# Kernel tuning notes

Hardware: AMD Instinct MI355X
Metric: run time of the kernel (lower is better)

The kernel has to match this reference:

```python
import math
import jax, jax.numpy as jnp
import numpy as np

V_NODES = 100000
N_EDGES = 1600000
EMBED = 768
HID = 256
H = 4
FH = HID // H
L = 2
PE_D = EMBED // 4  # 192
SLOPE = 0.2


def make_pe(max_len, d):
    pos = np.arange(max_len, dtype=np.float32)[:, None]
    div = np.exp(np.arange(0, d, 2, dtype=np.float32) * (-math.log(10000.0) / d))
    pe = np.zeros((max_len, d), dtype=np.float32)
    pe[:, 0::2] = np.sin(pos * div)
    pe[:, 1::2] = np.cos(pos * div)
    return jnp.asarray(pe)


def setup_inputs() -> dict:
    key = jax.random.key(0)
    ks = jax.random.split(key, 24)

    def xavier(k, shape):
        fan_in, fan_out = shape[0], shape[1]
        lim = math.sqrt(6.0 / (fan_in + fan_out))
        return jax.random.uniform(k, shape, jnp.float32, -lim, lim)

    in_proj_dim = EMBED + 2 * PE_D  # 1152
    inp = {
        'row_idx': jax.random.randint(ks[0], (V_NODES,), 0, 256),
        'col_idx': jax.random.randint(ks[1], (V_NODES,), 0, 64),
        'edge_index': jax.random.randint(ks[2], (2, N_EDGES), 0, V_NODES),
        'edge_weight': jax.random.uniform(ks[3], (N_EDGES,), jnp.float32),
        'W_in': xavier(ks[4], (in_proj_dim, HID)),
        'b_in': jnp.zeros((HID,), jnp.float32),
        'ln_g': jnp.ones((HID,), jnp.float32),
        'ln_b': jnp.zeros((HID,), jnp.float32),
        'Wq': jnp.stack([xavier(ks[5 + i], (HID, HID)) for i in range(L)]),
        'bq': jnp.zeros((L, HID), jnp.float32),
        'Wk': jnp.stack([xavier(ks[7 + i], (HID, HID)) for i in range(L)]),
        'bk': jnp.zeros((L, HID), jnp.float32),
        'Wv': jnp.stack([xavier(ks[9 + i], (HID, HID)) for i in range(L)]),
        'bv': jnp.zeros((L, HID), jnp.float32),
        'Wo': jnp.stack([xavier(ks[11 + i], (HID, HID)) for i in range(L)]),
        'bo': jnp.zeros((L, HID), jnp.float32),
        'We': jnp.stack([xavier(ks[13 + i], (1, H)) for i in range(L)]),  # edge_proj weight [1,H]
        'be': jnp.zeros((L, H), jnp.float32),
    }
    return inp


def gat_layer(h, src, tgt, ew, Wq, bq, Wk, bk, Wv, bv, Wo, bo, We, be):
    V = h.shape[0]
    Q = (h @ Wq + bq).reshape(V, H, FH)
    K = (h @ Wk + bk).reshape(V, H, FH)
    Vo = (h @ Wv + bv).reshape(V, H, FH)
    # edge bias: Linear(1,H) on edge_weight, then leaky relu -> [E,H]
    edge_bias = jax.nn.leaky_relu(ew[:, None] * We.reshape(1, H) + be, SLOPE)
    attn_raw = jnp.sum(Q[src] * K[tgt], axis=-1) / math.sqrt(FH) + edge_bias  # [E,H]
    attn_exp = jnp.exp(attn_raw)
    deg = jax.ops.segment_sum(attn_exp, tgt, num_segments=V) + 1e-16  # [V,H]
    attn_norm = attn_exp / deg[tgt]  # [E,H] (dropout is identity at eval)
    msg = Vo[src] * attn_norm[:, :, None] * ew[:, None, None]  # [E,H,FH]
    out = jax.ops.segment_sum(msg, tgt, num_segments=V).reshape(V, H * FH)
    return jax.nn.leaky_relu(out @ Wo + bo, SLOPE)


def reference(row_idx, col_idx, edge_index, edge_weight,
              W_in, b_in, ln_g, ln_b,
              Wq, bq, Wk, bk, Wv, bv, Wo, bo, We, be):
    V = row_idx.shape[0]
    row_pe = make_pe(256, PE_D)
    col_pe = make_pe(64, PE_D)
    cell = jnp.zeros((V, EMBED), jnp.float32)  # cell_embeds are zeros in source
    h = jnp.concatenate([cell, row_pe[row_idx], col_pe[col_idx]], axis=-1)
    # input_proj: Linear -> LayerNorm -> ReLU (dropout identity)
    h = h @ W_in + b_in
    mu = jnp.mean(h, axis=-1, keepdims=True)
    var = jnp.var(h, axis=-1, keepdims=True)
    h = (h - mu) / jnp.sqrt(var + 1e-5) * ln_g + ln_b
    h = jax.nn.relu(h)
    src, tgt = edge_index[0], edge_index[1]
    for i in range(L):
        h = gat_layer(h, src, tgt, edge_weight,
                      Wq[i], bq[i], Wk[i], bk[i], Wv[i], bv[i],
                      Wo[i], bo[i], We[i], be[i])
    return h
```

## Files before the change

### kernel.cpp

```cpp
#include <hip/hip_runtime.h>
#include <hip/hip_bf16.h>
#include <type_traits>
#include <math.h>

typedef __attribute__((ext_vector_type(8))) short bf16x8;
typedef __attribute__((ext_vector_type(4))) float f32x4;

__device__ __forceinline__ float bf2f(unsigned int u16) {
    union { unsigned int i; float f; } x; x.i = (u16 & 0xffffu) << 16; return x.f;
}
__device__ __forceinline__ unsigned int f2bf(float f) {
    union { float f; unsigned int i; } x; x.f = f;
    unsigned int i = x.i;
    unsigned int r = i + 0x7fffu + ((i >> 16) & 1u);
    return r >> 16;
}

#define SLOPE 0.2f

__global__ void k_hist(const int* __restrict__ tgt, int* __restrict__ cnt, int E) {
    int i = blockIdx.x * blockDim.x + threadIdx.x;
    if (i < E) atomicAdd(&cnt[tgt[i]], 1);
}

__global__ void __launch_bounds__(1024) k_scan1(const int* __restrict__ in, int* __restrict__ out,
                                                int* __restrict__ bsums, int n) {
    __shared__ int sm[1024];
    int i = blockIdx.x * 1024 + threadIdx.x;
    int v = (i < n) ? in[i] : 0;
    sm[threadIdx.x] = v; __syncthreads();
    for (int ofs = 1; ofs < 1024; ofs <<= 1) {
        int t = (threadIdx.x >= ofs) ? sm[threadIdx.x - ofs] : 0;
        __syncthreads();
        sm[threadIdx.x] += t;
        __syncthreads();
    }
    if (i < n) out[i] = sm[threadIdx.x];
    if (threadIdx.x == 1023) bsums[blockIdx.x] = sm[1023];
}

__global__ void __launch_bounds__(1024) k_scan2(int* bsums, int nb) {
    __shared__ int sm[1024];
    int v = (threadIdx.x < nb) ? bsums[threadIdx.x] : 0;
    sm[threadIdx.x] = v; __syncthreads();
    for (int ofs = 1; ofs < 1024; ofs <<= 1) {
        int t = (threadIdx.x >= ofs) ? sm[threadIdx.x - ofs] : 0;
        __syncthreads();
        sm[threadIdx.x] += t;
        __syncthreads();
    }
    if (threadIdx.x < nb) bsums[threadIdx.x] = sm[threadIdx.x] - v;
}

__global__ void __launch_bounds__(1024) k_scan3(int* __restrict__ out1, const int* __restrict__ bsums,
                                                int* __restrict__ off0, int n) {
    int i = blockIdx.x * 1024 + threadIdx.x;
    if (i < n) out1[i] += bsums[blockIdx.x];
    if (i == 0) off0[0] = 0;
}

__global__ void k_scatter(const int* __restrict__ ei, const float* __restrict__ ew,
                          const int* __restrict__ off, int* __restrict__ fill,
                          int* __restrict__ ssrc, float* __restrict__ sew, int E) {
    int e = blockIdx.x * blockDim.x + threadIdx.x;
    if (e < E) {
        int s = ei[e], t = ei[E + e];
        int pos = off[t] + atomicAdd(&fill[t], 1);
        ssrc[pos] = s; sew[pos] = ew[e];
    }
}

__global__ void k_combo(const int* __restrict__ ri, const int* __restrict__ ci,
                        int* __restrict__ combo, int V) {
    int v = blockIdx.x * blockDim.x + threadIdx.x;
    if (v < V) combo[v] = ri[v] * 64 + ci[v];
}

__global__ void __launch_bounds__(256) k_wt(const float* __restrict__ Wq, const float* __restrict__ Wk,
                                            const float* __restrict__ Wv, const float* __restrict__ Wo,
                                            unsigned short* __restrict__ WT) {
    __shared__ float sm[64][65];
    int blk = blockIdx.x;
    int m = blk >> 4, t = blk & 15;
    int tr = t >> 2, tc = t & 3;
    const float* srcs[4] = {Wq, Wk, Wv, Wo};
    const float* W = srcs[m & 3] + (size_t)(m >> 2) * 65536;
    int tid = threadIdx.x;
    for (int i = tid; i < 4096; i += 256) {
        int r = i >> 6, c = i & 63;
        sm[r][c] = W[(size_t)(tr * 64 + r) * 256 + tc * 64 + c];
    }
    __syncthreads();
    for (int i = tid; i < 4096; i += 256) {
        int n = i >> 6, k = i & 63;
        WT[(size_t)(m * 256 + tc * 64 + n) * 256 + tr * 64 + k] = (unsigned short)f2bf(sm[k][n]);
    }
}

__global__ void __launch_bounds__(256) k_bias(const float* __restrict__ bq, const float* __restrict__ bk,
                                              const float* __restrict__ bv, const float* __restrict__ bo,
                                              float* __restrict__ biasF) {
    int m = blockIdx.x, n = threadIdx.x;
    const float* srcs[4] = {bq, bk, bv, bo};
    biasF[m * 256 + n] = srcs[m & 3][(m >> 2) * 256 + n];
}

__global__ void __launch_bounds__(256) k_peproj(const float* __restrict__ W_in, float* __restrict__ AB) {
    __shared__ float pe[192];
    int blk = blockIdx.x;
    bool isA = blk < 256;
    int pos = isA ? blk : blk - 256;
    const float* Wb = W_in + (size_t)(isA ? 768 : 960) * 256;
    int tid = threadIdx.x;
    if (tid < 192) {
        float div = expf(-(float)(tid & ~1) * (logf(10000.0f) / 192.0f));
        float ang = (float)pos * div;
        pe[tid] = (tid & 1) ? cosf(ang) : sinf(ang);
    }
    __syncthreads();
    float acc = 0.f;
    #pragma unroll 8
    for (int d = 0; d < 192; ++d) acc = fmaf(pe[d], Wb[d * 256 + tid], acc);
    AB[blk * 256 + tid] = acc;
}

__global__ void __launch_bounds__(256) k_h0(const float* __restrict__ AB, const float* __restrict__ b_in,
                                            const float* __restrict__ g, const float* __restrict__ b,
                                            unsigned short* __restrict__ h0t) {
    int wid = threadIdx.x >> 6, lane = threadIdx.x & 63;
    int m = blockIdx.x * 4 + wid;
    int r = m >> 6, c = m & 63;
    float4 a  = ((const float4*)(AB + (size_t)r * 256))[lane];
    float4 bb = ((const float4*)(AB + (size_t)(256 + c) * 256))[lane];
    float4 bi = ((const float4*)b_in)[lane];
    float x0 = a.x + bb.x + bi.x, x1 = a.y + bb.y + bi.y;
    float x2 = a.z + bb.z + bi.z, x3 = a.w + bb.w + bi.w;
    float s = x0 + x1 + x2 + x3;
    #pragma unroll
    for (int msk = 1; msk < 64; msk <<= 1) s += __shfl_xor(s, msk);
    float mu = s * (1.f / 256.f);
    float d0 = x0 - mu, d1 = x1 - mu, d2 = x2 - mu, d3 = x3 - mu;
    float sq = d0 * d0 + d1 * d1 + d2 * d2 + d3 * d3;
    #pragma unroll
    for (int msk = 1; msk < 64; msk <<= 1) sq += __shfl_xor(sq, msk);
    float rstd = rsqrtf(sq * (1.f / 256.f) + 1e-5f);
    float4 gv = ((const float4*)g)[lane], bv = ((const float4*)b)[lane];
    float y0 = fmaxf(fmaf(d0 * rstd, gv.x, bv.x), 0.f);
    float y1 = fmaxf(fmaf(d1 * rstd, gv.y, bv.y), 0.f);
    float y2 = fmaxf(fmaf(d2 * rstd, gv.z, bv.z), 0.f);
    float y3 = fmaxf(fmaf(d3 * rstd, gv.w, bv.w), 0.f);
    uint2 o;
    o.x = f2bf(y0) | (f2bf(y1) << 16);
    o.y = f2bf(y2) | (f2bf(y3) << 16);
    *(uint2*)(h0t + (size_t)m * 256 + lane * 4) = o;
}

template <typename TC, bool LEAKY>
__global__ void __launch_bounds__(256) k_mm(const unsigned short* __restrict__ A,
                                            const unsigned short* __restrict__ WT,
                                            const float* __restrict__ bias,
                                            TC* __restrict__ C, int M, int ldc) {
    __shared__ __align__(16) unsigned short As[128][72];
    __shared__ __align__(16) unsigned short Bs[128][72];
    int tid = threadIdx.x;
    int R0 = blockIdx.x * 128, C0 = blockIdx.y * 128;
    int lane = tid & 63, wave = tid >> 6;
    int wr = (wave >> 1) * 64, wc = (wave & 1) * 64;
    int fr = lane & 15, fq = lane >> 4;
    f32x4 acc[4][4] = {};
    for (int k0 = 0; k0 < 256; k0 += 64) {
        for (int i = tid; i < 1024; i += 256) {
            int r = i >> 3, c8 = (i & 7) * 8;
            int gr = R0 + r;
            uint4 u = make_uint4(0u, 0u, 0u, 0u);
            if (gr < M) u = *(const uint4*)(A + (size_t)gr * 256 + k0 + c8);
            *(uint4*)&As[r][c8] = u;
            *(uint4*)&Bs[r][c8] = *(const uint4*)(WT + (size_t)(C0 + r) * 256 + k0 + c8);
        }
        __syncthreads();
        #pragma unroll
        for (int ks = 0; ks < 64; ks += 32) {
            bf16x8 af[4], bfv[4];
            #pragma unroll
            for (int mi = 0; mi < 4; ++mi) af[mi] = *(const bf16x8*)&As[wr + mi * 16 + fr][ks + fq * 8];
            #pragma unroll
            for (int ni = 0; ni < 4; ++ni) bfv[ni] = *(const bf16x8*)&Bs[wc + ni * 16 + fr][ks + fq * 8];
            #pragma unroll
            for (int mi = 0; mi < 4; ++mi)
                #pragma unroll
                for (int ni = 0; ni < 4; ++ni)
                    acc[mi][ni] = __builtin_amdgcn_mfma_f32_16x16x32_bf16(af[mi], bfv[ni], acc[mi][ni], 0, 0, 0);
        }
        __syncthreads();
    }
    #pragma unroll
    for (int mi = 0; mi < 4; ++mi) {
        #pragma unroll
        for (int r = 0; r < 4; ++r) {
            int row = R0 + wr + mi * 16 + fq * 4 + r;
            if (row >= M) continue;
            #pragma unroll
            for (int ni = 0; ni < 4; ++ni) {
                int col = C0 + wc + ni * 16 + fr;
                float v = acc[mi][ni][r] + bias[col];
                if (LEAKY) v = v > 0.f ? v : SLOPE * v;
                if constexpr (std::is_same<TC, float>::value) {
                    C[(size_t)row * ldc + col] = v;
                } else {
                    C[(size_t)row * ldc + col] = (unsigned short)f2bf(v);
                }
            }
        }
    }
}

template <bool USE_COMBO>
__global__ void __launch_bounds__(256) k_edge(const int* __restrict__ off, const int* __restrict__ ssrc,
                                              const float* __restrict__ sew, const int* __restrict__ combo,
                                              const unsigned short* __restrict__ QKV,
                                              const float* __restrict__ We_l, const float* __restrict__ be_l,
                                              unsigned short* __restrict__ out, int V) {
    int wid = threadIdx.x >> 6, lane = threadIdx.x & 63;
    int t = blockIdx.x * 4 + wid;
    if (t >= V) return;
    int h = lane >> 4;
    int krow = USE_COMBO ? combo[t] : t;
    uint2 ku = *(const uint2*)(QKV + (size_t)krow * 768 + 256 + lane * 4);
    float k0 = bf2f(ku.x), k1 = bf2f(ku.x >> 16), k2 = bf2f(ku.y), k3 = bf2f(ku.y >> 16);
    float Weh = We_l[h], beh = be_l[h];
    float n0 = 0.f, n1 = 0.f, n2 = 0.f, n3 = 0.f, den = 0.f;
    int beg = off[t], end = off[t + 1];
    for (int e0 = beg; e0 < end; e0 += 64) {
        int nrem = end - e0; if (nrem > 64) nrem = 64;
        int sv = 0; float wv = 0.f;
        if (lane < nrem) {
            sv = ssrc[e0 + lane];
            wv = sew[e0 + lane];
            if (USE_COMBO) sv = combo[sv];
        }
        for (int i = 0; i < nrem; ++i) {
            int srow = __shfl(sv, i);
            float w = __shfl(wv, i);
            uint2 qu = *(const uint2*)(QKV + (size_t)srow * 768 + lane * 4);
            float p = bf2f(qu.x) * k0 + bf2f(qu.x >> 16) * k1 + bf2f(qu.y) * k2 + bf2f(qu.y >> 16) * k3;
            p += __shfl_xor(p, 1);
            p += __shfl_xor(p, 2);
            p += __shfl_xor(p, 4);
            p += __shfl_xor(p, 8);
            float bias = fmaf(w, Weh, beh);
            bias = bias > 0.f ? bias : SLOPE * bias;
            float ex = expf(fmaf(p, 0.125f, bias));
            den += ex;
            float cc = ex * w;
            uint2 vu = *(const uint2*)(QKV + (size_t)srow * 768 + 512 + lane * 4);
            n0 = fmaf(cc, bf2f(vu.x), n0);
            n1 = fmaf(cc, bf2f(vu.x >> 16), n1);
            n2 = fmaf(cc, bf2f(vu.y), n2);
            n3 = fmaf(cc, bf2f(vu.y >> 16), n3);
        }
    }
    float inv = 1.f / (den + 1e-16f);
    uint2 o;
    o.x = f2bf(n0 * inv) | (f2bf(n1 * inv) << 16);
    o.y = f2bf(n2 * inv) | (f2bf(n3 * inv) << 16);
    *(uint2*)(out + (size_t)t * 256 + lane * 4) = o;
}

extern "C" void kernel_launch(void* const* d_in, const int* in_sizes, int n_in,
                              void* d_out, int out_size, void* d_ws, size_t ws_size,
                              hipStream_t stream) {
    const int*   row_idx = (const int*)d_in[0];
    const int*   col_idx = (const int*)d_in[1];
    const int*   ei      = (const int*)d_in[2];
    const float* ew      = (const float*)d_in[3];
    const float* W_in    = (const float*)d_in[4];
    const float* b_in    = (const float*)d_in[5];
    const float* ln_g    = (const float*)d_in[6];
    const float* ln_b    = (const float*)d_in[7];
    const float* Wq      = (const float*)d_in[8];
    const float* bq      = (const float*)d_in[9];
    const float* Wk      = (const float*)d_in[10];
    const float* bk      = (const float*)d_in[11];
    const float* Wv      = (const float*)d_in[12];
    const float* bv      = (const float*)d_in[13];
    const float* Wo      = (const float*)d_in[14];
    const float* bo      = (const float*)d_in[15];
    const float* We      = (const float*)d_in[16];
    const float* be      = (const float*)d_in[17];

    const int V = in_sizes[0];
    const int E = in_sizes[3];
    const int NC = 16384;

    char* w = (char*)d_ws;
    size_t o = 0;
    auto alloc = [&](size_t bytes) -> char* {
        char* p = w + o;
        o = (o + bytes + 255) & ~(size_t)255;
        return p;
    };
    int*   cnt     = (int*)alloc((size_t)V * 4);
    int*   fill    = (int*)alloc((size_t)V * 4);
    int*   csr_off = (int*)alloc((size_t)(V + 1) * 4);
    int*   bsums   = (int*)alloc(1024 * 4);
    int*   csr_src = (int*)alloc((size_t)E * 4);
    float* csr_ew  = (float*)alloc((size_t)E * 4);
    int*   combo   = (int*)alloc((size_t)V * 4);
    float* AB      = (float*)alloc((size_t)320 * 256 * 4);
    unsigned short* WT    = (unsigned short*)alloc((size_t)2048 * 256 * 2);
    float*          biasF = (float*)alloc((size_t)2048 * 4);
    unsigned short* h0t   = (unsigned short*)alloc((size_t)NC * 256 * 2);
    unsigned short* QKV1  = (unsigned short*)alloc((size_t)NC * 768 * 2);
    unsigned short* out_e = (unsigned short*)alloc((size_t)V * 256 * 2);
    unsigned short* h1    = (unsigned short*)alloc((size_t)V * 256 * 2);
    unsigned short* QKV2  = (unsigned short*)alloc((size_t)V * 768 * 2);

    hipMemsetAsync(cnt, 0, (size_t)V * 4, stream);
    hipMemsetAsync(fill, 0, (size_t)V * 4, stream);

    int eb = (E + 255) / 256;
    int nscan = (V + 1023) / 1024;
    k_hist<<<eb, 256, 0, stream>>>(ei + E, cnt, E);
    k_scan1<<<nscan, 1024, 0, stream>>>(cnt, csr_off + 1, bsums, V);
    k_scan2<<<1, 1024, 0, stream>>>(bsums, nscan);
    k_scan3<<<nscan, 1024, 0, stream>>>(csr_off + 1, bsums, csr_off, V);
    k_scatter<<<eb, 256, 0, stream>>>(ei, ew, csr_off, fill, csr_src, csr_ew, E);
    k_combo<<<(V + 255) / 256, 256, 0, stream>>>(row_idx, col_idx, combo, V);

    k_wt<<<128, 256, 0, stream>>>(Wq, Wk, Wv, Wo, WT);
    k_bias<<<8, 256, 0, stream>>>(bq, bk, bv, bo, biasF);
    k_peproj<<<320, 256, 0, stream>>>(W_in, AB);
    k_h0<<<NC / 4, 256, 0, stream>>>(AB, b_in, ln_g, ln_b, h0t);

    dim3 g1(NC / 128, 6);
    k_mm<unsigned short, false><<<g1, 256, 0, stream>>>(h0t, WT, biasF, QKV1, NC, 768);

    int tb = (V + 3) / 4;
    k_edge<true><<<tb, 256, 0, stream>>>(csr_off, csr_src, csr_ew, combo, QKV1, We, be, out_e, V);

    int mb = (V + 127) / 128;
    dim3 gо(mb, 2);
    dim3 gqkv(mb, 6);
    k_mm<unsigned short, true><<<gо, 256, 0, stream>>>(out_e, WT + (size_t)768 * 256, biasF + 768, h1, V, 256);
    k_mm<unsigned short, false><<<gqkv, 256, 0, stream>>>(h1, WT + (size_t)1024 * 256, biasF + 1024, QKV2, V, 768);

    k_edge<false><<<tb, 256, 0, stream>>>(csr_off, csr_src, csr_ew, combo, QKV2, We + 4, be + 4, out_e, V);

    k_mm<float, true><<<gо, 256, 0, stream>>>(out_e, WT + (size_t)1792 * 256, biasF + 1792, (float*)d_out, V, 256);
}
```

Baseline: 874.3 us.

## Process four edges per wavefront concurrently in edge attention kernel

Restructures the per-target edge kernel so that each quarter-wave of 16 lanes handles a different edge. Each lane loads 16 bf16 values with 128-bit loads instead of 4 with 64-bit loads. The change shortens the serial per-edge loop, shrinks the cross-lane dot-product reduction, and uses __expf in place of expf. In exchange it adds a final cross-quarter reduction of 17 values, raises register use to 16 accumulators and 16 K values per lane, and wastes lanes when a node's degree is not a multiple of four. Leaky ReLU is also rewritten as fmaxf, and a misnamed grid variable is fixed.

After: 861.1 us. No clear change (-1.5%).

```diff
diff --git a/kernel.cpp b/kernel.cpp
--- a/kernel.cpp
+++ b/kernel.cpp
@@ -203,7 +203,7 @@
             for (int ni = 0; ni < 4; ++ni) {
                 int col = C0 + wc + ni * 16 + fr;
                 float v = acc[mi][ni][r] + bias[col];
-                if (LEAKY) v = v > 0.f ? v : SLOPE * v;
+                if (LEAKY) v = fmaxf(v, SLOPE * v);
                 if constexpr (std::is_same<TC, float>::value) {
                     C[(size_t)row * ldc + col] = v;
                 } else {
@@ -223,12 +223,21 @@
     int wid = threadIdx.x >> 6, lane = threadIdx.x & 63;
     int t = blockIdx.x * 4 + wid;
     if (t >= V) return;
-    int h = lane >> 4;
+    int q = lane & 15, quarter = lane >> 4;
+    int h = q >> 2;
     int krow = USE_COMBO ? combo[t] : t;
-    uint2 ku = *(const uint2*)(QKV + (size_t)krow * 768 + 256 + lane * 4);
-    float k0 = bf2f(ku.x), k1 = bf2f(ku.x >> 16), k2 = bf2f(ku.y), k3 = bf2f(ku.y >> 16);
+    uint4 ka = *(const uint4*)(QKV + (size_t)krow * 768 + 256 + q * 16);
+    uint4 kb = *(const uint4*)(QKV + (size_t)krow * 768 + 256 + q * 16 + 8);
+    float kf[16];
+    kf[0] = bf2f(ka.x); kf[1] = bf2f(ka.x >> 16); kf[2] = bf2f(ka.y); kf[3] = bf2f(ka.y >> 16);
+    kf[4] = bf2f(ka.z); kf[5] = bf2f(ka.z >> 16); kf[6] = bf2f(ka.w); kf[7] = bf2f(ka.w >> 16);
+    kf[8] = bf2f(kb.x); kf[9] = bf2f(kb.x >> 16); kf[10] = bf2f(kb.y); kf[11] = bf2f(kb.y >> 16);
+    kf[12] = bf2f(kb.z); kf[13] = bf2f(kb.z >> 16); kf[14] = bf2f(kb.w); kf[15] = bf2f(kb.w >> 16);
     float Weh = We_l[h], beh = be_l[h];
-    float n0 = 0.f, n1 = 0.f, n2 = 0.f, n3 = 0.f, den = 0.f;
+    float n[16];
+    #pragma unroll
+    for (int j = 0; j < 16; ++j) n[j] = 0.f;
+    float den = 0.f;
     int beg = off[t], end = off[t + 1];
     for (int e0 = beg; e0 < end; e0 += 64) {
         int nrem = end - e0; if (nrem > 64) nrem = 64;
@@ -238,32 +247,80 @@
             wv = sew[e0 + lane];
             if (USE_COMBO) sv = combo[sv];
         }
-        for (int i = 0; i < nrem; ++i) {
-            int srow = __shfl(sv, i);
-            float w = __shfl(wv, i);
-            uint2 qu = *(const uint2*)(QKV + (size_t)srow * 768 + lane * 4);
-            float p = bf2f(qu.x) * k0 + bf2f(qu.x >> 16) * k1 + bf2f(qu.y) * k2 + bf2f(qu.y >> 16) * k3;
+        for (int i = 0; i < nrem; i += 4) {
+            int ei = i + quarter;
+            bool act = ei < nrem;
+            int eidx = act ? ei : (nrem - 1);
+            int srow = __shfl(sv, eidx);
+            float w  = __shfl(wv, eidx);
+            const unsigned short* base = QKV + (size_t)srow * 768 + q * 16;
+            uint4 qa = *(const uint4*)base;
+            uint4 qb = *(const uint4*)(base + 8);
+            uint4 va = *(const uint4*)(base + 512);
+            uint4 vb = *(const uint4*)(base + 520);
+            float p;
+            p = bf2f(qa.x) * kf[0];
+            p = fmaf(bf2f(qa.x >> 16), kf[1], p);
+            p = fmaf(bf2f(qa.y),       kf[2], p);
+            p = fmaf(bf2f(qa.y >> 16), kf[3], p);
+            p = fmaf(bf2f(qa.z),       kf[4], p);
+            p = fmaf(bf2f(qa.z >> 16), kf[5], p);
+            p = fmaf(bf2f(qa.w),       kf[6], p);
+            p = fmaf(bf2f(qa.w >> 16), kf[7], p);
+            p = fmaf(bf2f(qb.x),       kf[8], p);
+            p = fmaf(bf2f(qb.x >> 16), kf[9], p);
+            p = fmaf(bf2f(qb.y),       kf[10], p);
+            p = fmaf(bf2f(qb.y >> 16), kf[11], p);
+            p = fmaf(bf2f(qb.z),       kf[12], p);
+            p = fmaf(bf2f(qb.z >> 16), kf[13], p);
+            p = fmaf(bf2f(qb.w),       kf[14], p);
+            p = fmaf(bf2f(qb.w >> 16), kf[15], p);
             p += __shfl_xor(p, 1);
             p += __shfl_xor(p, 2);
-            p += __shfl_xor(p, 4);
-            p += __shfl_xor(p, 8);
             float bias = fmaf(w, Weh, beh);
-            bias = bias > 0.f ? bias : SLOPE * bias;
-            float ex = expf(fmaf(p, 0.125f, bias));
+            bias = fmaxf(bias, SLOPE * bias);
+            float ex = act ? __expf(fmaf(p, 0.125f, bias)) : 0.f;
             den += ex;
             float cc = ex * w;
-            uint2 vu = *(const uint2*)(QKV + (size_t)srow * 768 + 512 + lane * 4);
-            n0 = fmaf(cc, bf2f(vu.x), n0);
-            n1 = fmaf(cc, bf2f(vu.x >> 16), n1);
-            n2 = fmaf(cc, bf2f(vu.y), n2);
-            n3 = fmaf(cc, bf2f(vu.y >> 16), n3);
+            n[0]  = fmaf(cc, bf2f(va.x),       n[0]);
+            n[1]  = fmaf(cc, bf2f(va.x >> 16), n[1]);
+            n[2]  = fmaf(cc, bf2f(va.y),       n[2]);
+            n[3]  = fmaf(cc, bf2f(va.y >> 16), n[3]);
+            n[4]  = fmaf(cc, bf2f(va.z),       n[4]);
+            n[5]  = fmaf(cc, bf2f(va.z >> 16), n[5]);
+            n[6]  = fmaf(cc, bf2f(va.w),       n[6]);
+            n[7]  = fmaf(cc, bf2f(va.w >> 16), n[7]);
+            n[8]  = fmaf(cc, bf2f(vb.x),       n[8]);
+            n[9]  = fmaf(cc, bf2f(vb.x >> 16), n[9]);
+            n[10] = fmaf(cc, bf2f(vb.y),       n[10]);
+            n[11] = fmaf(cc, bf2f(vb.y >> 16), n[11]);
+            n[12] = fmaf(cc, bf2f(vb.z),       n[12]);
+            n[13] = fmaf(cc, bf2f(vb.z >> 16), n[13]);
+            n[14] = fmaf(cc, bf2f(vb.w),       n[14]);
+            n[15] = fmaf(cc, bf2f(vb.w >> 16), n[15]);
         }
     }
+    den += __shfl_xor(den, 16);
+    den += __shfl_xor(den, 32);
+    #pragma unroll
+    for (int j = 0; j < 16; ++j) {
+        n[j] += __shfl_xor(n[j], 16);
+        n[j] += __shfl_xor(n[j], 32);
+    }
     float inv = 1.f / (den + 1e-16f);
-    uint2 o;
-    o.x = f2bf(n0 * inv) | (f2bf(n1 * inv) << 16);
-    o.y = f2bf(n2 * inv) | (f2bf(n3 * inv) << 16);
-    *(uint2*)(out + (size_t)t * 256 + lane * 4) = o;
+    if (quarter == 0) {
+        uint4 o0, o1;
+        o0.x = f2bf(n[0] * inv)  | (f2bf(n[1] * inv) << 16);
+        o0.y = f2bf(n[2] * inv)  | (f2bf(n[3] * inv) << 16);
+        o0.z = f2bf(n[4] * inv)  | (f2bf(n[5] * inv) << 16);
+        o0.w = f2bf(n[6] * inv)  | (f2bf(n[7] * inv) << 16);
+        o1.x = f2bf(n[8] * inv)  | (f2bf(n[9] * inv) << 16);
+        o1.y = f2bf(n[10] * inv) | (f2bf(n[11] * inv) << 16);
+        o1.z = f2bf(n[12] * inv) | (f2bf(n[13] * inv) << 16);
+        o1.w = f2bf(n[14] * inv) | (f2bf(n[15] * inv) << 16);
+        *(uint4*)(out + (size_t)t * 256 + q * 16) = o0;
+        *(uint4*)(out + (size_t)t * 256 + q * 16 + 8) = o1;
+    }
 }
 
 extern "C" void kernel_launch(void* const* d_in, const int* in_sizes, int n_in,
@@ -339,12 +396,12 @@
     k_edge<true><<<tb, 256, 0, stream>>>(csr_off, csr_src, csr_ew, combo, QKV1, We, be, out_e, V);
 
     int mb = (V + 127) / 128;
-    dim3 gо(mb, 2);
+    dim3 go(mb, 2);
     dim3 gqkv(mb, 6);
-    k_mm<unsigned short, true><<<gо, 256, 0, stream>>>(out_e, WT + (size_t)768 * 256, biasF + 768, h1, V, 256);
+    k_mm<unsigned short, true><<<go, 256, 0, stream>>>(out_e, WT + (size_t)768 * 256, biasF + 768, h1, V, 256);
     k_mm<unsigned short, false><<<gqkv, 256, 0, stream>>>(h1, WT + (size_t)1024 * 256, biasF + 1024, QKV2, V, 768);
 
     k_edge<false><<<tb, 256, 0, stream>>>(csr_off, csr_src, csr_ew, combo, QKV2, We + 4, be + 4, out_e, V);
 
-    k_mm<float, true><<<gо, 256, 0, stream>>>(out_e, WT + (size_t)1792 * 256, biasF + 1792, (float*)d_out, V, 256);
-}
+    k_mm<float, true><<<go, 256, 0, stream>>>(out_e, WT + (size_t)1792 * 256, biasF + 1792, (float*)d_out, V, 256);
+}
```
